# Performance work log

Hardware: AMD Instinct MI355X
Metric: run time of the kernel (lower is better)

Reference implementation:

```python
import jax, jax.numpy as jnp
import numpy as np

EPS_ROT = 1e-6
EPS_FRAME = 1e-8


def make_rotX(angs):
    # angs: [..., 2] (cos-like, sin-like); returns [..., 4, 4]
    n = jnp.sqrt(jnp.sum(angs * angs, axis=-1)) + EPS_ROT
    c = angs[..., 0] / n
    s = angs[..., 1] / n
    z = jnp.zeros_like(c)
    o = jnp.ones_like(c)
    rows = jnp.stack([o, z, z, z,
                      z, c, -s, z,
                      z, s, c, z,
                      z, z, z, o], axis=-1)
    return rows.reshape(c.shape + (4, 4))


def make_rotZ(angs):
    n = jnp.sqrt(jnp.sum(angs * angs, axis=-1)) + EPS_ROT
    c = angs[..., 0] / n
    s = angs[..., 1] / n
    z = jnp.zeros_like(c)
    o = jnp.ones_like(c)
    rows = jnp.stack([c, -s, z, z,
                      s, c, z, z,
                      z, z, o, z,
                      z, z, z, o], axis=-1)
    return rows.reshape(c.shape + (4, 4))


def make_rot_axis(angs, u):
    # Rodrigues rotation about unit axis u, as homogeneous 4x4
    n = jnp.sqrt(jnp.sum(angs * angs, axis=-1)) + EPS_ROT
    ct = angs[..., 0] / n
    st = angs[..., 1] / n
    u0, u1, u2 = u[..., 0], u[..., 1], u[..., 2]
    omc = 1.0 - ct
    z = jnp.zeros_like(ct)
    o = jnp.ones_like(ct)
    rows = jnp.stack([
        ct + u0 * u0 * omc, u0 * u1 * omc - u2 * st, u0 * u2 * omc + u1 * st, z,
        u0 * u1 * omc + u2 * st, ct + u1 * u1 * omc, u1 * u2 * omc - u0 * st, z,
        u0 * u2 * omc - u1 * st, u1 * u2 * omc + u0 * st, ct + u2 * u2 * omc, z,
        z, z, z, o], axis=-1)
    return rows.reshape(ct.shape + (4, 4))


def rigid_from_3_points(N, Ca, C):
    # Gram-Schmidt backbone frame (ideal geometry branch)
    v1 = C - Ca
    v2 = N - Ca
    e1 = v1 / (jnp.linalg.norm(v1, axis=-1, keepdims=True) + EPS_FRAME)
    u2 = v2 - e1 * jnp.sum(e1 * v2, axis=-1, keepdims=True)
    e2 = u2 / (jnp.linalg.norm(u2, axis=-1, keepdims=True) + EPS_FRAME)
    e3 = jnp.cross(e1, e2)
    R = jnp.stack([e1, e2, e3], axis=-1)  # columns -> [B,L,3,3]
    return R, Ca


def _compute(seq, xyz, alphas, base_indices, RTs_in_base_frame, xyzs_in_base_frame):
    B, L = xyz.shape[:2]
    Rs, Ts = rigid_from_3_points(xyz[..., 0, :], xyz[..., 1, :], xyz[..., 2, :])
    top = jnp.concatenate([Rs, Ts[..., None]], axis=-1)  # [B,L,3,4]
    bot = jnp.broadcast_to(jnp.array([0.0, 0.0, 0.0, 1.0], dtype=xyz.dtype), (B, L, 1, 4))
    RTF0 = jnp.concatenate([top, bot], axis=-2)  # [B,L,4,4]

    RT_base = RTs_in_base_frame[seq]  # [B,L,7,4,4]

    RTF1 = RTF0 @ RT_base[:, :, 0] @ make_rotX(alphas[:, :, 0, :])
    RTF2 = RTF0 @ RT_base[:, :, 1] @ make_rotX(alphas[:, :, 1, :])
    RTF3 = RTF0 @ RT_base[:, :, 2] @ make_rotX(alphas[:, :, 2, :])

    basexyzs = xyzs_in_base_frame[seq]  # [B,L,36,4]
    NCr = 0.5 * (basexyzs[:, :, 2, :3] + basexyzs[:, :, 0, :3])
    CAr = basexyzs[:, :, 1, :3]
    CBr = basexyzs[:, :, 4, :3]
    ax1 = jnp.cross(CBr - CAr, NCr - CAr)
    ax1 = ax1 / (jnp.linalg.norm(ax1, axis=-1, keepdims=True) + 1e-8)
    NCp = basexyzs[:, :, 2, :3] - basexyzs[:, :, 0, :3]
    NCpp = NCp - jnp.sum(NCp * NCr, axis=-1, keepdims=True) / jnp.sum(NCr * NCr, axis=-1, keepdims=True) * NCr
    ax2 = jnp.cross(CBr - CAr, NCpp)
    ax2 = ax2 / (jnp.linalg.norm(ax2, axis=-1, keepdims=True) + 1e-8)

    CBrot1 = make_rot_axis(alphas[:, :, 7, :], ax1)
    CBrot2 = make_rot_axis(alphas[:, :, 8, :], ax2)
    RTF8 = RTF0 @ CBrot1 @ CBrot2

    RTF4 = RTF8 @ RT_base[:, :, 3] @ make_rotX(alphas[:, :, 3, :]) @ make_rotZ(alphas[:, :, 9, :])
    RTF5 = RTF4 @ RT_base[:, :, 4] @ make_rotX(alphas[:, :, 4, :])
    RTF6 = RTF5 @ RT_base[:, :, 5] @ make_rotX(alphas[:, :, 5, :])
    RTF7 = RTF6 @ RT_base[:, :, 6] @ make_rotX(alphas[:, :, 6, :])

    RTframes = jnp.stack([RTF0, RTF1, RTF2, RTF3, RTF4, RTF5, RTF6, RTF7, RTF8], axis=2)  # [B,L,9,4,4]

    idx = base_indices[seq]  # [B,L,36], values in [0,9)
    frames = jnp.take_along_axis(RTframes, idx[..., None, None], axis=2)  # [B,L,36,4,4]
    xyzs = jnp.einsum('blaij,blaj->blai', frames, basexyzs)
    return RTframes, xyzs[..., :3]


def setup_inputs() -> dict:
    key = jax.random.key(0)
    ks = jax.random.split(key, 6)
    B, L, NAA, NATOMS = 4, 8192, 80, 36
    seq = jax.random.randint(ks[0], (B, L), 0, NAA)
    xyz = jax.random.normal(ks[1], (B, L, 3, 3), jnp.float32)
    alphas = jax.random.normal(ks[2], (B, L, 10, 2), jnp.float32)
    base_indices = jax.random.randint(ks[3], (NAA, NATOMS), 0, 9)
    xibf = jax.random.normal(ks[4], (NAA, NATOMS, 4), jnp.float32)
    xibf = xibf.at[..., 3].set(1.0)  # homogeneous coords
    RTs = jax.random.normal(ks[5], (NAA, 7, 4, 4), jnp.float32)
    return {"seq": seq, "xyz": xyz, "alphas": alphas, "base_indices": base_indices,
            "RTs_in_base_frame": RTs, "xyzs_in_base_frame": xibf}


def reference(seq, xyz, alphas, base_indices, RTs_in_base_frame, xyzs_in_base_frame):
    return _compute(seq, xyz, alphas, base_indices, RTs_in_base_frame, xyzs_in_base_frame)
```

## Files before the change

kernel.cpp:

```cpp
#include <hip/hip_runtime.h>

#define RPB 64
#define FRS 20
#define RSS (9*FRS)


__device__ __forceinline__ float rsqz(float d) { return rsqrtf(fmaxf(d, 1e-24f)); }

__device__ __forceinline__ void angNorm(float x, float y, float& c, float& s) {
    float inv = rsqz(x*x + y*y);
    c = x * inv; s = y * inv;
}

__device__ __forceinline__ float4 rowMat(const float4 f, const float* __restrict__ B) {
    const float4* q = reinterpret_cast<const float4*>(B);
    float4 b0 = q[0], b1 = q[1], b2 = q[2], b3 = q[3];
    float4 o;
    o.x = f.x*b0.x + f.y*b1.x + f.z*b2.x + f.w*b3.x;
    o.y = f.x*b0.y + f.y*b1.y + f.z*b2.y + f.w*b3.y;
    o.z = f.x*b0.z + f.y*b1.z + f.z*b2.z + f.w*b3.z;
    o.w = f.x*b0.w + f.y*b1.w + f.z*b2.w + f.w*b3.w;
    return o;
}

__device__ __forceinline__ void rotXrow(float4& v, float c, float s) {
    float v1 = v.y, v2 = v.z;
    v.y = c*v1 + s*v2;
    v.z = c*v2 - s*v1;
}

__device__ __forceinline__ void rotZrow(float4& v, float c, float s) {
    float v0 = v.x, v1 = v.y;
    v.x = c*v0 + s*v1;
    v.y = c*v1 - s*v0;
}

__device__ __forceinline__ float4 applyG(const float4 f, const float G[3][3]) {
    float4 o;
    o.x = f.x*G[0][0] + f.y*G[1][0] + f.z*G[2][0];
    o.y = f.x*G[0][1] + f.y*G[1][1] + f.z*G[2][1];
    o.z = f.x*G[0][2] + f.y*G[1][2] + f.z*G[2][2];
    o.w = f.w;
    return o;
}

__device__ __forceinline__ void rotAxis3(float G[3][3], float c, float s,
                                         float u0, float u1, float u2) {
    float omc = 1.0f - c;
    G[0][0] = c + u0*u0*omc;    G[0][1] = u0*u1*omc - u2*s; G[0][2] = u0*u2*omc + u1*s;
    G[1][0] = u0*u1*omc + u2*s; G[1][1] = c + u1*u1*omc;    G[1][2] = u1*u2*omc - u0*s;
    G[2][0] = u0*u2*omc - u1*s; G[2][1] = u1*u2*omc + u0*s; G[2][2] = c + u2*u2*omc;
}


__global__ __launch_bounds__(256, 2) void fused_kernel(
    const int*   __restrict__ seq,
    const float* __restrict__ xyz,
    const float* __restrict__ alphas,
    const int*   __restrict__ bidx,
    const float* __restrict__ RTs,
    const float* __restrict__ xibf,
    float*       __restrict__ out_fr,
    float*       __restrict__ out_xyz,
    int BL)
{
    __shared__ __align__(16) float lds_fr[RPB * RSS];
    __shared__ int lds_seq[RPB];

    const int tid   = threadIdx.x;
    const int lane  = tid & 63;
    const int wv    = tid >> 6;
    const int i     = lane & 3;
    const int res   = wv*16 + (lane >> 2);
    const int base  = blockIdx.x * RPB;
    const int t     = base + res;
    const bool valid = (t < BL);

    float* fl = lds_fr + res * RSS;
    float* fg = out_fr + (size_t)t * 144;

    if (valid) {
        int s = seq[t];
        if (i == 0) lds_seq[res] = s;
        const float* rb = RTs + (size_t)s * 112;
        const float* al = alphas + (size_t)t * 20;

        const float* p = xyz + (size_t)t * 9;
        float N0=p[0], N1=p[1], N2=p[2];
        float A0=p[3], A1=p[4], A2=p[5];
        float C0=p[6], C1=p[7], C2=p[8];
        float v10=C0-A0, v11=C1-A1, v12=C2-A2;
        float v20=N0-A0, v21=N1-A1, v22=N2-A2;
        float i1 = rsqz(v10*v10 + v11*v11 + v12*v12);
        float e10=v10*i1, e11=v11*i1, e12=v12*i1;
        float d  = e10*v20 + e11*v21 + e12*v22;
        float u20=v20-e10*d, u21=v21-e11*d, u22=v22-e12*d;
        float i2 = rsqz(u20*u20 + u21*u21 + u22*u22);
        float e20=u20*i2, e21=u21*i2, e22=u22*i2;
        float e30=e11*e22 - e12*e21;
        float e31=e12*e20 - e10*e22;
        float e32=e10*e21 - e11*e20;

        bool s0 = (i==0), s1 = (i==1), s2 = (i==2);
        float4 f0r;
        f0r.x = s0?e10 : s1?e11 : s2?e12 : 0.f;
        f0r.y = s0?e20 : s1?e21 : s2?e22 : 0.f;
        f0r.z = s0?e30 : s1?e31 : s2?e32 : 0.f;
        f0r.w = s0?A0  : s1?A1  : s2?A2  : 1.f;

        *reinterpret_cast<float4*>(fl + i*4) = f0r;
        *reinterpret_cast<float4*>(fg + i*4) = f0r;

        const float4* a4p = reinterpret_cast<const float4*>(al);
        float4 q0 = a4p[0], q1 = a4p[1], q2 = a4p[2], q3 = a4p[3], q4 = a4p[4];
        float ca0,sa0, ca1,sa1, ca2,sa2, ca3,sa3, ca4,sa4;
        float ca5,sa5, ca6,sa6, ca7,sa7, ca8,sa8, ca9,sa9;
        angNorm(q0.x,q0.y, ca0,sa0);  angNorm(q0.z,q0.w, ca1,sa1);
        angNorm(q1.x,q1.y, ca2,sa2);  angNorm(q1.z,q1.w, ca3,sa3);
        angNorm(q2.x,q2.y, ca4,sa4);  angNorm(q2.z,q2.w, ca5,sa5);
        angNorm(q3.x,q3.y, ca6,sa6);  angNorm(q3.z,q3.w, ca7,sa7);
        angNorm(q4.x,q4.y, ca8,sa8);  angNorm(q4.z,q4.w, ca9,sa9);

        float4 rw;
        rw = rowMat(f0r, rb +  0); rotXrow(rw, ca0, sa0);
        *reinterpret_cast<float4*>(fl + 1*FRS + i*4) = rw;
        *reinterpret_cast<float4*>(fg + 16 + i*4) = rw;
        rw = rowMat(f0r, rb + 16); rotXrow(rw, ca1, sa1);
        *reinterpret_cast<float4*>(fl + 2*FRS + i*4) = rw;
        *reinterpret_cast<float4*>(fg + 32 + i*4) = rw;
        rw = rowMat(f0r, rb + 32); rotXrow(rw, ca2, sa2);
        *reinterpret_cast<float4*>(fl + 3*FRS + i*4) = rw;
        *reinterpret_cast<float4*>(fg + 48 + i*4) = rw;

        const float* bxp = xibf + (size_t)s * 144;
        float4 b0 = reinterpret_cast<const float4*>(bxp)[0];
        float4 b1 = reinterpret_cast<const float4*>(bxp)[1];
        float4 b2 = reinterpret_cast<const float4*>(bxp)[2];
        float4 b4 = reinterpret_cast<const float4*>(bxp)[4];

        float NCr0 = 0.5f*(b2.x + b0.x), NCr1 = 0.5f*(b2.y + b0.y), NCr2 = 0.5f*(b2.z + b0.z);
        float ba0 = b4.x - b1.x, ba1 = b4.y - b1.y, ba2 = b4.z - b1.z;
        float w0 = NCr0 - b1.x, w1 = NCr1 - b1.y, w2 = NCr2 - b1.z;
        float x10 = ba1*w2 - ba2*w1, x11 = ba2*w0 - ba0*w2, x12 = ba0*w1 - ba1*w0;
        float in1 = rsqz(x10*x10 + x11*x11 + x12*x12);
        x10 *= in1; x11 *= in1; x12 *= in1;
        float NCp0 = b2.x - b0.x, NCp1 = b2.y - b0.y, NCp2 = b2.z - b0.z;
        float dp = NCp0*NCr0 + NCp1*NCr1 + NCp2*NCr2;
        float dr = NCr0*NCr0 + NCr1*NCr1 + NCr2*NCr2;
        float sf = dp / dr;
        float g0 = NCp0 - sf*NCr0, g1 = NCp1 - sf*NCr1, g2 = NCp2 - sf*NCr2;
        float x20 = ba1*g2 - ba2*g1, x21 = ba2*g0 - ba0*g2, x22 = ba0*g1 - ba1*g0;
        float in2 = rsqz(x20*x20 + x21*x21 + x22*x22);
        x20 *= in2; x21 *= in2; x22 *= in2;

        float G1[3][3], G2[3][3];
        rotAxis3(G1, ca7, sa7, x10, x11, x12);
        rotAxis3(G2, ca8, sa8, x20, x21, x22);

        float4 f8r = applyG(applyG(f0r, G1), G2);
        *reinterpret_cast<float4*>(fl + 8*FRS + i*4) = f8r;
        *reinterpret_cast<float4*>(fg + 128 + i*4) = f8r;

        rw = rowMat(f8r, rb + 48); rotXrow(rw, ca3, sa3); rotZrow(rw, ca9, sa9);
        *reinterpret_cast<float4*>(fl + 4*FRS + i*4) = rw;
        *reinterpret_cast<float4*>(fg + 64 + i*4) = rw;
        rw = rowMat(rw, rb + 64); rotXrow(rw, ca4, sa4);
        *reinterpret_cast<float4*>(fl + 5*FRS + i*4) = rw;
        *reinterpret_cast<float4*>(fg + 80 + i*4) = rw;
        rw = rowMat(rw, rb + 80); rotXrow(rw, ca5, sa5);
        *reinterpret_cast<float4*>(fl + 6*FRS + i*4) = rw;
        *reinterpret_cast<float4*>(fg + 96 + i*4) = rw;
        rw = rowMat(rw, rb + 96); rotXrow(rw, ca6, sa6);
        *reinterpret_cast<float4*>(fl + 7*FRS + i*4) = rw;
        *reinterpret_cast<float4*>(fg + 112 + i*4) = rw;
    }

    const int wbase = wv * 16;
#pragma unroll
    for (int k = 0; k < 9; ++k) {
        int c = k*64 + lane;
        int lres = c / 36;
        int a = c - lres*36;
        int res2 = wbase + lres;
        int tt = base + res2;
        if (tt < BL) {
            int ss  = lds_seq[res2];
            int idx = bidx[ss*36 + a];
            float4 v = *reinterpret_cast<const float4*>(xibf + ((size_t)ss*36 + a)*4);
            const float* fp = lds_fr + res2*RSS + idx*FRS;
            float4 r0 = *reinterpret_cast<const float4*>(fp);
            float4 r1 = *reinterpret_cast<const float4*>(fp + 4);
            float4 r2 = *reinterpret_cast<const float4*>(fp + 8);
            size_t o = ((size_t)(base + wbase)*36 + c)*3;
            out_xyz[o+0] = r0.x*v.x + r0.y*v.y + r0.z*v.z + r0.w*v.w;
            out_xyz[o+1] = r1.x*v.x + r1.y*v.y + r1.z*v.z + r1.w*v.w;
            out_xyz[o+2] = r2.x*v.x + r2.y*v.y + r2.z*v.z + r2.w*v.w;
        }
    }
}


extern "C" void kernel_launch(void* const* d_in, const int* in_sizes, int n_in,
                              void* d_out, int out_size, void* d_ws, size_t ws_size,
                              hipStream_t stream) {
    const int*   seq    = (const int*)  d_in[0];
    const float* xyz    = (const float*)d_in[1];
    const float* alphas = (const float*)d_in[2];
    const int*   bidx   = (const int*)  d_in[3];
    const float* RTs    = (const float*)d_in[4];
    const float* xibf   = (const float*)d_in[5];
    float*       out    = (float*)d_out;

    int BL = in_sizes[0];
    float* out_xyz = out + (size_t)BL * 144;

    int blocks = (BL + RPB - 1) / RPB;
    fused_kernel<<<blocks, 256, 0, stream>>>(seq, xyz, alphas, bidx, RTs, xibf,
                                             out, out_xyz, BL);
}
```

Measured before the change: 14.53 us.

## Split fused kernel into separate frames and atoms kernels

Breaks the single fused kernel into two launches. The first computes the nine frames per residue and writes them to global memory. The second reads those frames back from global memory (mostly L2) to transform the 36 atoms, one thread per atom. This drops the large LDS staging buffer that limited occupancy and the uneven atom loop, at the cost of an extra launch and a round-trip of the frame data through memory.

```diff
diff --git a/kernel.cpp b/kernel.cpp
--- a/kernel.cpp
+++ b/kernel.cpp
@@ -1,8 +1,4 @@
 #include <hip/hip_runtime.h>
-
-#define RPB 64
-#define FRS 20
-#define RSS (9*FRS)
 
 
 __device__ __forceinline__ float rsqz(float d) { return rsqrtf(fmaxf(d, 1e-24f)); }
@@ -53,150 +49,133 @@
 }
 
 
-__global__ __launch_bounds__(256, 2) void fused_kernel(
+__global__ __launch_bounds__(256, 2) void frames_kernel(
     const int*   __restrict__ seq,
     const float* __restrict__ xyz,
     const float* __restrict__ alphas,
-    const int*   __restrict__ bidx,
     const float* __restrict__ RTs,
     const float* __restrict__ xibf,
     float*       __restrict__ out_fr,
+    int BL)
+{
+    const int tid  = blockIdx.x * 256 + threadIdx.x;
+    const int i    = tid & 3;
+    const int t    = tid >> 2;
+    if (t >= BL) return;
+
+    int s = seq[t];
+    const float* rb = RTs + (size_t)s * 112;
+    const float* al = alphas + (size_t)t * 20;
+    float* fg = out_fr + (size_t)t * 144;
+
+    const float* p = xyz + (size_t)t * 9;
+    float N0=p[0], N1=p[1], N2=p[2];
+    float A0=p[3], A1=p[4], A2=p[5];
+    float C0=p[6], C1=p[7], C2=p[8];
+    float v10=C0-A0, v11=C1-A1, v12=C2-A2;
+    float v20=N0-A0, v21=N1-A1, v22=N2-A2;
+    float i1 = rsqz(v10*v10 + v11*v11 + v12*v12);
+    float e10=v10*i1, e11=v11*i1, e12=v12*i1;
+    float d  = e10*v20 + e11*v21 + e12*v22;
+    float u20=v20-e10*d, u21=v21-e11*d, u22=v22-e12*d;
+    float i2 = rsqz(u20*u20 + u21*u21 + u22*u22);
+    float e20=u20*i2, e21=u21*i2, e22=u22*i2;
+    float e30=e11*e22 - e12*e21;
+    float e31=e12*e20 - e10*e22;
+    float e32=e10*e21 - e11*e20;
+
+    bool s0 = (i==0), s1 = (i==1), s2 = (i==2);
+    float4 f0r;
+    f0r.x = s0?e10 : s1?e11 : s2?e12 : 0.f;
+    f0r.y = s0?e20 : s1?e21 : s2?e22 : 0.f;
+    f0r.z = s0?e30 : s1?e31 : s2?e32 : 0.f;
+    f0r.w = s0?A0  : s1?A1  : s2?A2  : 1.f;
+    *reinterpret_cast<float4*>(fg + i*4) = f0r;
+
+    const float4* a4p = reinterpret_cast<const float4*>(al);
+    float4 q0 = a4p[0], q1 = a4p[1], q2 = a4p[2], q3 = a4p[3], q4 = a4p[4];
+    float ca0,sa0, ca1,sa1, ca2,sa2, ca3,sa3, ca4,sa4;
+    float ca5,sa5, ca6,sa6, ca7,sa7, ca8,sa8, ca9,sa9;
+    angNorm(q0.x,q0.y, ca0,sa0);  angNorm(q0.z,q0.w, ca1,sa1);
+    angNorm(q1.x,q1.y, ca2,sa2);  angNorm(q1.z,q1.w, ca3,sa3);
+    angNorm(q2.x,q2.y, ca4,sa4);  angNorm(q2.z,q2.w, ca5,sa5);
+    angNorm(q3.x,q3.y, ca6,sa6);  angNorm(q3.z,q3.w, ca7,sa7);
+    angNorm(q4.x,q4.y, ca8,sa8);  angNorm(q4.z,q4.w, ca9,sa9);
+
+    float4 rw;
+    rw = rowMat(f0r, rb +  0); rotXrow(rw, ca0, sa0);
+    *reinterpret_cast<float4*>(fg + 16 + i*4) = rw;
+    rw = rowMat(f0r, rb + 16); rotXrow(rw, ca1, sa1);
+    *reinterpret_cast<float4*>(fg + 32 + i*4) = rw;
+    rw = rowMat(f0r, rb + 32); rotXrow(rw, ca2, sa2);
+    *reinterpret_cast<float4*>(fg + 48 + i*4) = rw;
+
+    const float* bxp = xibf + (size_t)s * 144;
+    float4 b0 = reinterpret_cast<const float4*>(bxp)[0];
+    float4 b1 = reinterpret_cast<const float4*>(bxp)[1];
+    float4 b2 = reinterpret_cast<const float4*>(bxp)[2];
+    float4 b4 = reinterpret_cast<const float4*>(bxp)[4];
+
+    float NCr0 = 0.5f*(b2.x + b0.x), NCr1 = 0.5f*(b2.y + b0.y), NCr2 = 0.5f*(b2.z + b0.z);
+    float ba0 = b4.x - b1.x, ba1 = b4.y - b1.y, ba2 = b4.z - b1.z;
+    float w0 = NCr0 - b1.x, w1 = NCr1 - b1.y, w2 = NCr2 - b1.z;
+    float x10 = ba1*w2 - ba2*w1, x11 = ba2*w0 - ba0*w2, x12 = ba0*w1 - ba1*w0;
+    float in1 = rsqz(x10*x10 + x11*x11 + x12*x12);
+    x10 *= in1; x11 *= in1; x12 *= in1;
+    float NCp0 = b2.x - b0.x, NCp1 = b2.y - b0.y, NCp2 = b2.z - b0.z;
+    float dp = NCp0*NCr0 + NCp1*NCr1 + NCp2*NCr2;
+    float dr = NCr0*NCr0 + NCr1*NCr1 + NCr2*NCr2;
+    float sf = dp / dr;
+    float g0 = NCp0 - sf*NCr0, g1 = NCp1 - sf*NCr1, g2 = NCp2 - sf*NCr2;
+    float x20 = ba1*g2 - ba2*g1, x21 = ba2*g0 - ba0*g2, x22 = ba0*g1 - ba1*g0;
+    float in2 = rsqz(x20*x20 + x21*x21 + x22*x22);
+    x20 *= in2; x21 *= in2; x22 *= in2;
+
+    float G1[3][3], G2[3][3];
+    rotAxis3(G1, ca7, sa7, x10, x11, x12);
+    rotAxis3(G2, ca8, sa8, x20, x21, x22);
+
+    float4 f8r = applyG(applyG(f0r, G1), G2);
+    *reinterpret_cast<float4*>(fg + 128 + i*4) = f8r;
+
+    rw = rowMat(f8r, rb + 48); rotXrow(rw, ca3, sa3); rotZrow(rw, ca9, sa9);
+    *reinterpret_cast<float4*>(fg + 64 + i*4) = rw;
+    rw = rowMat(rw, rb + 64); rotXrow(rw, ca4, sa4);
+    *reinterpret_cast<float4*>(fg + 80 + i*4) = rw;
+    rw = rowMat(rw, rb + 80); rotXrow(rw, ca5, sa5);
+    *reinterpret_cast<float4*>(fg + 96 + i*4) = rw;
+    rw = rowMat(rw, rb + 96); rotXrow(rw, ca6, sa6);
+    *reinterpret_cast<float4*>(fg + 112 + i*4) = rw;
+}
+
+
+__global__ __launch_bounds__(256) void atoms_kernel(
+    const int*   __restrict__ seq,
+    const int*   __restrict__ bidx,
+    const float* __restrict__ xibf,
+    const float* __restrict__ frames,
     float*       __restrict__ out_xyz,
     int BL)
 {
-    __shared__ __align__(16) float lds_fr[RPB * RSS];
-    __shared__ int lds_seq[RPB];
-
-    const int tid   = threadIdx.x;
-    const int lane  = tid & 63;
-    const int wv    = tid >> 6;
-    const int i     = lane & 3;
-    const int res   = wv*16 + (lane >> 2);
-    const int base  = blockIdx.x * RPB;
-    const int t     = base + res;
-    const bool valid = (t < BL);
-
-    float* fl = lds_fr + res * RSS;
-    float* fg = out_fr + (size_t)t * 144;
-
-    if (valid) {
-        int s = seq[t];
-        if (i == 0) lds_seq[res] = s;
-        const float* rb = RTs + (size_t)s * 112;
-        const float* al = alphas + (size_t)t * 20;
-
-        const float* p = xyz + (size_t)t * 9;
-        float N0=p[0], N1=p[1], N2=p[2];
-        float A0=p[3], A1=p[4], A2=p[5];
-        float C0=p[6], C1=p[7], C2=p[8];
-        float v10=C0-A0, v11=C1-A1, v12=C2-A2;
-        float v20=N0-A0, v21=N1-A1, v22=N2-A2;
-        float i1 = rsqz(v10*v10 + v11*v11 + v12*v12);
-        float e10=v10*i1, e11=v11*i1, e12=v12*i1;
-        float d  = e10*v20 + e11*v21 + e12*v22;
-        float u20=v20-e10*d, u21=v21-e11*d, u22=v22-e12*d;
-        float i2 = rsqz(u20*u20 + u21*u21 + u22*u22);
-        float e20=u20*i2, e21=u21*i2, e22=u22*i2;
-        float e30=e11*e22 - e12*e21;
-        float e31=e12*e20 - e10*e22;
-        float e32=e10*e21 - e11*e20;
-
-        bool s0 = (i==0), s1 = (i==1), s2 = (i==2);
-        float4 f0r;
-        f0r.x = s0?e10 : s1?e11 : s2?e12 : 0.f;
-        f0r.y = s0?e20 : s1?e21 : s2?e22 : 0.f;
-        f0r.z = s0?e30 : s1?e31 : s2?e32 : 0.f;
-        f0r.w = s0?A0  : s1?A1  : s2?A2  : 1.f;
-
-        *reinterpret_cast<float4*>(fl + i*4) = f0r;
-        *reinterpret_cast<float4*>(fg + i*4) = f0r;
-
-        const float4* a4p = reinterpret_cast<const float4*>(al);
-        float4 q0 = a4p[0], q1 = a4p[1], q2 = a4p[2], q3 = a4p[3], q4 = a4p[4];
-        float ca0,sa0, ca1,sa1, ca2,sa2, ca3,sa3, ca4,sa4;
-        float ca5,sa5, ca6,sa6, ca7,sa7, ca8,sa8, ca9,sa9;
-        angNorm(q0.x,q0.y, ca0,sa0);  angNorm(q0.z,q0.w, ca1,sa1);
-        angNorm(q1.x,q1.y, ca2,sa2);  angNorm(q1.z,q1.w, ca3,sa3);
-        angNorm(q2.x,q2.y, ca4,sa4);  angNorm(q2.z,q2.w, ca5,sa5);
-        angNorm(q3.x,q3.y, ca6,sa6);  angNorm(q3.z,q3.w, ca7,sa7);
-        angNorm(q4.x,q4.y, ca8,sa8);  angNorm(q4.z,q4.w, ca9,sa9);
-
-        float4 rw;
-        rw = rowMat(f0r, rb +  0); rotXrow(rw, ca0, sa0);
-        *reinterpret_cast<float4*>(fl + 1*FRS + i*4) = rw;
-        *reinterpret_cast<float4*>(fg + 16 + i*4) = rw;
-        rw = rowMat(f0r, rb + 16); rotXrow(rw, ca1, sa1);
-        *reinterpret_cast<float4*>(fl + 2*FRS + i*4) = rw;
-        *reinterpret_cast<float4*>(fg + 32 + i*4) = rw;
-        rw = rowMat(f0r, rb + 32); rotXrow(rw, ca2, sa2);
-        *reinterpret_cast<float4*>(fl + 3*FRS + i*4) = rw;
-        *reinterpret_cast<float4*>(fg + 48 + i*4) = rw;
-
-        const float* bxp = xibf + (size_t)s * 144;
-        float4 b0 = reinterpret_cast<const float4*>(bxp)[0];
-        float4 b1 = reinterpret_cast<const float4*>(bxp)[1];
-        float4 b2 = reinterpret_cast<const float4*>(bxp)[2];
-        float4 b4 = reinterpret_cast<const float4*>(bxp)[4];
-
-        float NCr0 = 0.5f*(b2.x + b0.x), NCr1 = 0.5f*(b2.y + b0.y), NCr2 = 0.5f*(b2.z + b0.z);
-        float ba0 = b4.x - b1.x, ba1 = b4.y - b1.y, ba2 = b4.z - b1.z;
-        float w0 = NCr0 - b1.x, w1 = NCr1 - b1.y, w2 = NCr2 - b1.z;
-        float x10 = ba1*w2 - ba2*w1, x11 = ba2*w0 - ba0*w2, x12 = ba0*w1 - ba1*w0;
-        float in1 = rsqz(x10*x10 + x11*x11 + x12*x12);
-        x10 *= in1; x11 *= in1; x12 *= in1;
-        float NCp0 = b2.x - b0.x, NCp1 = b2.y - b0.y, NCp2 = b2.z - b0.z;
-        float dp = NCp0*NCr0 + NCp1*NCr1 + NCp2*NCr2;
-        float dr = NCr0*NCr0 + NCr1*NCr1 + NCr2*NCr2;
-        float sf = dp / dr;
-        float g0 = NCp0 - sf*NCr0, g1 = NCp1 - sf*NCr1, g2 = NCp2 - sf*NCr2;
-        float x20 = ba1*g2 - ba2*g1, x21 = ba2*g0 - ba0*g2, x22 = ba0*g1 - ba1*g0;
-        float in2 = rsqz(x20*x20 + x21*x21 + x22*x22);
-        x20 *= in2; x21 *= in2; x22 *= in2;
-
-        float G1[3][3], G2[3][3];
-        rotAxis3(G1, ca7, sa7, x10, x11, x12);
-        rotAxis3(G2, ca8, sa8, x20, x21, x22);
-
-        float4 f8r = applyG(applyG(f0r, G1), G2);
-        *reinterpret_cast<float4*>(fl + 8*FRS + i*4) = f8r;
-        *reinterpret_cast<float4*>(fg + 128 + i*4) = f8r;
-
-        rw = rowMat(f8r, rb + 48); rotXrow(rw, ca3, sa3); rotZrow(rw, ca9, sa9);
-        *reinterpret_cast<float4*>(fl + 4*FRS + i*4) = rw;
-        *reinterpret_cast<float4*>(fg + 64 + i*4) = rw;
-        rw = rowMat(rw, rb + 64); rotXrow(rw, ca4, sa4);
-        *reinterpret_cast<float4*>(fl + 5*FRS + i*4) = rw;
-        *reinterpret_cast<float4*>(fg + 80 + i*4) = rw;
-        rw = rowMat(rw, rb + 80); rotXrow(rw, ca5, sa5);
-        *reinterpret_cast<float4*>(fl + 6*FRS + i*4) = rw;
-        *reinterpret_cast<float4*>(fg + 96 + i*4) = rw;
-        rw = rowMat(rw, rb + 96); rotXrow(rw, ca6, sa6);
-        *reinterpret_cast<float4*>(fl + 7*FRS + i*4) = rw;
-        *reinterpret_cast<float4*>(fg + 112 + i*4) = rw;
-    }
-
-    const int wbase = wv * 16;
-#pragma unroll
-    for (int k = 0; k < 9; ++k) {
-        int c = k*64 + lane;
-        int lres = c / 36;
-        int a = c - lres*36;
-        int res2 = wbase + lres;
-        int tt = base + res2;
-        if (tt < BL) {
-            int ss  = lds_seq[res2];
-            int idx = bidx[ss*36 + a];
-            float4 v = *reinterpret_cast<const float4*>(xibf + ((size_t)ss*36 + a)*4);
-            const float* fp = lds_fr + res2*RSS + idx*FRS;
-            float4 r0 = *reinterpret_cast<const float4*>(fp);
-            float4 r1 = *reinterpret_cast<const float4*>(fp + 4);
-            float4 r2 = *reinterpret_cast<const float4*>(fp + 8);
-            size_t o = ((size_t)(base + wbase)*36 + c)*3;
-            out_xyz[o+0] = r0.x*v.x + r0.y*v.y + r0.z*v.z + r0.w*v.w;
-            out_xyz[o+1] = r1.x*v.x + r1.y*v.y + r1.z*v.z + r1.w*v.w;
-            out_xyz[o+2] = r2.x*v.x + r2.y*v.y + r2.z*v.z + r2.w*v.w;
-        }
-    }
+    int g = blockIdx.x * 256 + threadIdx.x;
+    if (g >= BL * 36) return;
+    int t = g / 36;
+    int a = g - t * 36;
+    int s = seq[t];
+    int idx = bidx[s * 36 + a];
+
+    const float4* fr = reinterpret_cast<const float4*>(frames + ((size_t)t * 9 + idx) * 16);
+    float4 r0 = fr[0], r1 = fr[1], r2 = fr[2];
+    float4 v  = *reinterpret_cast<const float4*>(xibf + ((size_t)s * 36 + a) * 4);
+
+    float x = r0.x*v.x + r0.y*v.y + r0.z*v.z + r0.w*v.w;
+    float y = r1.x*v.x + r1.y*v.y + r1.z*v.z + r1.w*v.w;
+    float z = r2.x*v.x + r2.y*v.y + r2.z*v.z + r2.w*v.w;
+
+    size_t o = (size_t)g * 3;
+    out_xyz[o+0] = x;
+    out_xyz[o+1] = y;
+    out_xyz[o+2] = z;
 }
 
 
@@ -214,7 +193,9 @@
     int BL = in_sizes[0];
     float* out_xyz = out + (size_t)BL * 144;
 
-    int blocks = (BL + RPB - 1) / RPB;
-    fused_kernel<<<blocks, 256, 0, stream>>>(seq, xyz, alphas, bidx, RTs, xibf,
-                                             out, out_xyz, BL);
-}
+    int blocksA = (BL * 4 + 255) / 256;
+    frames_kernel<<<blocksA, 256, 0, stream>>>(seq, xyz, alphas, RTs, xibf, out, BL);
+
+    int blocksB = (BL * 36 + 255) / 256;
+    atoms_kernel<<<blocksB, 256, 0, stream>>>(seq, bidx, xibf, out, out_xyz, BL);
+}
```

Result: slower. 23.66 us (+62.8%).

## Split block into frame-compute and gather-prefetch warps with block-wide sync

Applied to the files above, without the earlier changes.

Doubles the block to 512 threads. The first four waves compute residue frames into LDS and global memory, while the extra four waves prefetch base indices and base-frame coordinates for the atom stage. After a block-wide barrier, all 512 threads share the per-atom transform, so the index and coordinate loads can overlap the frame math. The cost is a __syncthreads that replaces the old per-wave independence, plus extra registers held by the prefetch waves.

```diff
diff --git a/kernel.cpp b/kernel.cpp
--- a/kernel.cpp
+++ b/kernel.cpp
@@ -53,7 +53,7 @@
 }
 
 
-__global__ __launch_bounds__(256, 2) void fused_kernel(
+__global__ __launch_bounds__(512, 4) void fused_kernel(
     const int*   __restrict__ seq,
     const float* __restrict__ xyz,
     const float* __restrict__ alphas,
@@ -67,134 +67,160 @@
     __shared__ __align__(16) float lds_fr[RPB * RSS];
     __shared__ int lds_seq[RPB];
 
-    const int tid   = threadIdx.x;
-    const int lane  = tid & 63;
-    const int wv    = tid >> 6;
-    const int i     = lane & 3;
-    const int res   = wv*16 + (lane >> 2);
-    const int base  = blockIdx.x * RPB;
-    const int t     = base + res;
-    const bool valid = (t < BL);
-
-    float* fl = lds_fr + res * RSS;
-    float* fg = out_fr + (size_t)t * 144;
-
-    if (valid) {
-        int s = seq[t];
-        if (i == 0) lds_seq[res] = s;
-        const float* rb = RTs + (size_t)s * 112;
-        const float* al = alphas + (size_t)t * 20;
-
-        const float* p = xyz + (size_t)t * 9;
-        float N0=p[0], N1=p[1], N2=p[2];
-        float A0=p[3], A1=p[4], A2=p[5];
-        float C0=p[6], C1=p[7], C2=p[8];
-        float v10=C0-A0, v11=C1-A1, v12=C2-A2;
-        float v20=N0-A0, v21=N1-A1, v22=N2-A2;
-        float i1 = rsqz(v10*v10 + v11*v11 + v12*v12);
-        float e10=v10*i1, e11=v11*i1, e12=v12*i1;
-        float d  = e10*v20 + e11*v21 + e12*v22;
-        float u20=v20-e10*d, u21=v21-e11*d, u22=v22-e12*d;
-        float i2 = rsqz(u20*u20 + u21*u21 + u22*u22);
-        float e20=u20*i2, e21=u21*i2, e22=u22*i2;
-        float e30=e11*e22 - e12*e21;
-        float e31=e12*e20 - e10*e22;
-        float e32=e10*e21 - e11*e20;
-
-        bool s0 = (i==0), s1 = (i==1), s2 = (i==2);
-        float4 f0r;
-        f0r.x = s0?e10 : s1?e11 : s2?e12 : 0.f;
-        f0r.y = s0?e20 : s1?e21 : s2?e22 : 0.f;
-        f0r.z = s0?e30 : s1?e31 : s2?e32 : 0.f;
-        f0r.w = s0?A0  : s1?A1  : s2?A2  : 1.f;
-
-        *reinterpret_cast<float4*>(fl + i*4) = f0r;
-        *reinterpret_cast<float4*>(fg + i*4) = f0r;
-
-        const float4* a4p = reinterpret_cast<const float4*>(al);
-        float4 q0 = a4p[0], q1 = a4p[1], q2 = a4p[2], q3 = a4p[3], q4 = a4p[4];
-        float ca0,sa0, ca1,sa1, ca2,sa2, ca3,sa3, ca4,sa4;
-        float ca5,sa5, ca6,sa6, ca7,sa7, ca8,sa8, ca9,sa9;
-        angNorm(q0.x,q0.y, ca0,sa0);  angNorm(q0.z,q0.w, ca1,sa1);
-        angNorm(q1.x,q1.y, ca2,sa2);  angNorm(q1.z,q1.w, ca3,sa3);
-        angNorm(q2.x,q2.y, ca4,sa4);  angNorm(q2.z,q2.w, ca5,sa5);
-        angNorm(q3.x,q3.y, ca6,sa6);  angNorm(q3.z,q3.w, ca7,sa7);
-        angNorm(q4.x,q4.y, ca8,sa8);  angNorm(q4.z,q4.w, ca9,sa9);
-
-        float4 rw;
-        rw = rowMat(f0r, rb +  0); rotXrow(rw, ca0, sa0);
-        *reinterpret_cast<float4*>(fl + 1*FRS + i*4) = rw;
-        *reinterpret_cast<float4*>(fg + 16 + i*4) = rw;
-        rw = rowMat(f0r, rb + 16); rotXrow(rw, ca1, sa1);
-        *reinterpret_cast<float4*>(fl + 2*FRS + i*4) = rw;
-        *reinterpret_cast<float4*>(fg + 32 + i*4) = rw;
-        rw = rowMat(f0r, rb + 32); rotXrow(rw, ca2, sa2);
-        *reinterpret_cast<float4*>(fl + 3*FRS + i*4) = rw;
-        *reinterpret_cast<float4*>(fg + 48 + i*4) = rw;
-
-        const float* bxp = xibf + (size_t)s * 144;
-        float4 b0 = reinterpret_cast<const float4*>(bxp)[0];
-        float4 b1 = reinterpret_cast<const float4*>(bxp)[1];
-        float4 b2 = reinterpret_cast<const float4*>(bxp)[2];
-        float4 b4 = reinterpret_cast<const float4*>(bxp)[4];
-
-        float NCr0 = 0.5f*(b2.x + b0.x), NCr1 = 0.5f*(b2.y + b0.y), NCr2 = 0.5f*(b2.z + b0.z);
-        float ba0 = b4.x - b1.x, ba1 = b4.y - b1.y, ba2 = b4.z - b1.z;
-        float w0 = NCr0 - b1.x, w1 = NCr1 - b1.y, w2 = NCr2 - b1.z;
-        float x10 = ba1*w2 - ba2*w1, x11 = ba2*w0 - ba0*w2, x12 = ba0*w1 - ba1*w0;
-        float in1 = rsqz(x10*x10 + x11*x11 + x12*x12);
-        x10 *= in1; x11 *= in1; x12 *= in1;
-        float NCp0 = b2.x - b0.x, NCp1 = b2.y - b0.y, NCp2 = b2.z - b0.z;
-        float dp = NCp0*NCr0 + NCp1*NCr1 + NCp2*NCr2;
-        float dr = NCr0*NCr0 + NCr1*NCr1 + NCr2*NCr2;
-        float sf = dp / dr;
-        float g0 = NCp0 - sf*NCr0, g1 = NCp1 - sf*NCr1, g2 = NCp2 - sf*NCr2;
-        float x20 = ba1*g2 - ba2*g1, x21 = ba2*g0 - ba0*g2, x22 = ba0*g1 - ba1*g0;
-        float in2 = rsqz(x20*x20 + x21*x21 + x22*x22);
-        x20 *= in2; x21 *= in2; x22 *= in2;
-
-        float G1[3][3], G2[3][3];
-        rotAxis3(G1, ca7, sa7, x10, x11, x12);
-        rotAxis3(G2, ca8, sa8, x20, x21, x22);
-
-        float4 f8r = applyG(applyG(f0r, G1), G2);
-        *reinterpret_cast<float4*>(fl + 8*FRS + i*4) = f8r;
-        *reinterpret_cast<float4*>(fg + 128 + i*4) = f8r;
-
-        rw = rowMat(f8r, rb + 48); rotXrow(rw, ca3, sa3); rotZrow(rw, ca9, sa9);
-        *reinterpret_cast<float4*>(fl + 4*FRS + i*4) = rw;
-        *reinterpret_cast<float4*>(fg + 64 + i*4) = rw;
-        rw = rowMat(rw, rb + 64); rotXrow(rw, ca4, sa4);
-        *reinterpret_cast<float4*>(fl + 5*FRS + i*4) = rw;
-        *reinterpret_cast<float4*>(fg + 80 + i*4) = rw;
-        rw = rowMat(rw, rb + 80); rotXrow(rw, ca5, sa5);
-        *reinterpret_cast<float4*>(fl + 6*FRS + i*4) = rw;
-        *reinterpret_cast<float4*>(fg + 96 + i*4) = rw;
-        rw = rowMat(rw, rb + 96); rotXrow(rw, ca6, sa6);
-        *reinterpret_cast<float4*>(fl + 7*FRS + i*4) = rw;
-        *reinterpret_cast<float4*>(fg + 112 + i*4) = rw;
+    const int tid  = threadIdx.x;
+    const int lane = tid & 63;
+    const int wv   = tid >> 6;
+    const int base = blockIdx.x * RPB;
+
+    int    pf_idx[5];
+    float4 pf_v[5];
+
+    if (wv < 4) {
+        const int i   = lane & 3;
+        const int res = wv*16 + (lane >> 2);
+        const int t   = base + res;
+        if (t < BL) {
+            int s = seq[t];
+            if (i == 0) lds_seq[res] = s;
+            const float* rb = RTs + (size_t)s * 112;
+            const float* al = alphas + (size_t)t * 20;
+            float* fl = lds_fr + res * RSS;
+            float* fg = out_fr + (size_t)t * 144;
+
+            const float* p = xyz + (size_t)t * 9;
+            float N0=p[0], N1=p[1], N2=p[2];
+            float A0=p[3], A1=p[4], A2=p[5];
+            float C0=p[6], C1=p[7], C2=p[8];
+            float v10=C0-A0, v11=C1-A1, v12=C2-A2;
+            float v20=N0-A0, v21=N1-A1, v22=N2-A2;
+            float i1 = rsqz(v10*v10 + v11*v11 + v12*v12);
+            float e10=v10*i1, e11=v11*i1, e12=v12*i1;
+            float d  = e10*v20 + e11*v21 + e12*v22;
+            float u20=v20-e10*d, u21=v21-e11*d, u22=v22-e12*d;
+            float i2 = rsqz(u20*u20 + u21*u21 + u22*u22);
+            float e20=u20*i2, e21=u21*i2, e22=u22*i2;
+            float e30=e11*e22 - e12*e21;
+            float e31=e12*e20 - e10*e22;
+            float e32=e10*e21 - e11*e20;
+
+            bool c0 = (i==0), c1 = (i==1), c2 = (i==2);
+            float4 f0r;
+            f0r.x = c0?e10 : c1?e11 : c2?e12 : 0.f;
+            f0r.y = c0?e20 : c1?e21 : c2?e22 : 0.f;
+            f0r.z = c0?e30 : c1?e31 : c2?e32 : 0.f;
+            f0r.w = c0?A0  : c1?A1  : c2?A2  : 1.f;
+            *reinterpret_cast<float4*>(fl + i*4) = f0r;
+            *reinterpret_cast<float4*>(fg + i*4) = f0r;
+
+            const float4* a4p = reinterpret_cast<const float4*>(al);
+            float4 q0 = a4p[0], q1 = a4p[1], q2 = a4p[2], q3 = a4p[3], q4 = a4p[4];
+            float ca0,sa0, ca1,sa1, ca2,sa2, ca3,sa3, ca4,sa4;
+            float ca5,sa5, ca6,sa6, ca7,sa7, ca8,sa8, ca9,sa9;
+            angNorm(q0.x,q0.y, ca0,sa0);  angNorm(q0.z,q0.w, ca1,sa1);
+            angNorm(q1.x,q1.y, ca2,sa2);  angNorm(q1.z,q1.w, ca3,sa3);
+            angNorm(q2.x,q2.y, ca4,sa4);  angNorm(q2.z,q2.w, ca5,sa5);
+            angNorm(q3.x,q3.y, ca6,sa6);  angNorm(q3.z,q3.w, ca7,sa7);
+            angNorm(q4.x,q4.y, ca8,sa8);  angNorm(q4.z,q4.w, ca9,sa9);
+
+            float4 rw;
+            rw = rowMat(f0r, rb +  0); rotXrow(rw, ca0, sa0);
+            *reinterpret_cast<float4*>(fl + 1*FRS + i*4) = rw;
+            *reinterpret_cast<float4*>(fg + 16 + i*4) = rw;
+            rw = rowMat(f0r, rb + 16); rotXrow(rw, ca1, sa1);
+            *reinterpret_cast<float4*>(fl + 2*FRS + i*4) = rw;
+            *reinterpret_cast<float4*>(fg + 32 + i*4) = rw;
+            rw = rowMat(f0r, rb + 32); rotXrow(rw, ca2, sa2);
+            *reinterpret_cast<float4*>(fl + 3*FRS + i*4) = rw;
+            *reinterpret_cast<float4*>(fg + 48 + i*4) = rw;
+
+            const float* bxp = xibf + (size_t)s * 144;
+            float4 b0 = reinterpret_cast<const float4*>(bxp)[0];
+            float4 b1 = reinterpret_cast<const float4*>(bxp)[1];
+            float4 b2 = reinterpret_cast<const float4*>(bxp)[2];
+            float4 b4 = reinterpret_cast<const float4*>(bxp)[4];
+
+            float NCr0 = 0.5f*(b2.x + b0.x), NCr1 = 0.5f*(b2.y + b0.y), NCr2 = 0.5f*(b2.z + b0.z);
+            float ba0 = b4.x - b1.x, ba1 = b4.y - b1.y, ba2 = b4.z - b1.z;
+            float w0 = NCr0 - b1.x, w1 = NCr1 - b1.y, w2 = NCr2 - b1.z;
+            float x10 = ba1*w2 - ba2*w1, x11 = ba2*w0 - ba0*w2, x12 = ba0*w1 - ba1*w0;
+            float in1 = rsqz(x10*x10 + x11*x11 + x12*x12);
+            x10 *= in1; x11 *= in1; x12 *= in1;
+            float NCp0 = b2.x - b0.x, NCp1 = b2.y - b0.y, NCp2 = b2.z - b0.z;
+            float dp = NCp0*NCr0 + NCp1*NCr1 + NCp2*NCr2;
+            float dr = NCr0*NCr0 + NCr1*NCr1 + NCr2*NCr2;
+            float sf = dp / dr;
+            float g0 = NCp0 - sf*NCr0, g1 = NCp1 - sf*NCr1, g2 = NCp2 - sf*NCr2;
+            float x20 = ba1*g2 - ba2*g1, x21 = ba2*g0 - ba0*g2, x22 = ba0*g1 - ba1*g0;
+            float in2 = rsqz(x20*x20 + x21*x21 + x22*x22);
+            x20 *= in2; x21 *= in2; x22 *= in2;
+
+            float G1[3][3], G2[3][3];
+            rotAxis3(G1, ca7, sa7, x10, x11, x12);
+            rotAxis3(G2, ca8, sa8, x20, x21, x22);
+
+            float4 f8r = applyG(applyG(f0r, G1), G2);
+            *reinterpret_cast<float4*>(fl + 8*FRS + i*4) = f8r;
+            *reinterpret_cast<float4*>(fg + 128 + i*4) = f8r;
+
+            rw = rowMat(f8r, rb + 48); rotXrow(rw, ca3, sa3); rotZrow(rw, ca9, sa9);
+            *reinterpret_cast<float4*>(fl + 4*FRS + i*4) = rw;
+            *reinterpret_cast<float4*>(fg + 64 + i*4) = rw;
+            rw = rowMat(rw, rb + 64); rotXrow(rw, ca4, sa4);
+            *reinterpret_cast<float4*>(fl + 5*FRS + i*4) = rw;
+            *reinterpret_cast<float4*>(fg + 80 + i*4) = rw;
+            rw = rowMat(rw, rb + 80); rotXrow(rw, ca5, sa5);
+            *reinterpret_cast<float4*>(fl + 6*FRS + i*4) = rw;
+            *reinterpret_cast<float4*>(fg + 96 + i*4) = rw;
+            rw = rowMat(rw, rb + 96); rotXrow(rw, ca6, sa6);
+            *reinterpret_cast<float4*>(fl + 7*FRS + i*4) = rw;
+            *reinterpret_cast<float4*>(fg + 112 + i*4) = rw;
+        }
+    } else {
+#pragma unroll
+        for (int k = 0; k < 5; ++k) {
+            int c = tid + k*512;
+            pf_idx[k] = 0;
+            pf_v[k] = make_float4(0.f, 0.f, 0.f, 0.f);
+            if (c < RPB*36) {
+                int res = c / 36;
+                int a = c - res*36;
+                int tt = base + res;
+                if (tt < BL) {
+                    int ss = seq[tt];
+                    pf_idx[k] = bidx[ss*36 + a];
+                    pf_v[k]   = *reinterpret_cast<const float4*>(xibf + ((size_t)ss*36 + a)*4);
+                }
+            }
+        }
     }
-
-    const int wbase = wv * 16;
+    __syncthreads();
+
 #pragma unroll
-    for (int k = 0; k < 9; ++k) {
-        int c = k*64 + lane;
-        int lres = c / 36;
-        int a = c - lres*36;
-        int res2 = wbase + lres;
-        int tt = base + res2;
-        if (tt < BL) {
-            int ss  = lds_seq[res2];
-            int idx = bidx[ss*36 + a];
-            float4 v = *reinterpret_cast<const float4*>(xibf + ((size_t)ss*36 + a)*4);
-            const float* fp = lds_fr + res2*RSS + idx*FRS;
-            float4 r0 = *reinterpret_cast<const float4*>(fp);
-            float4 r1 = *reinterpret_cast<const float4*>(fp + 4);
-            float4 r2 = *reinterpret_cast<const float4*>(fp + 8);
-            size_t o = ((size_t)(base + wbase)*36 + c)*3;
-            out_xyz[o+0] = r0.x*v.x + r0.y*v.y + r0.z*v.z + r0.w*v.w;
-            out_xyz[o+1] = r1.x*v.x + r1.y*v.y + r1.z*v.z + r1.w*v.w;
-            out_xyz[o+2] = r2.x*v.x + r2.y*v.y + r2.z*v.z + r2.w*v.w;
+    for (int k = 0; k < 5; ++k) {
+        int c = tid + k*512;
+        if (c < RPB*36) {
+            int res = c / 36;
+            int a = c - res*36;
+            int tt = base + res;
+            if (tt < BL) {
+                int idx; float4 v;
+                if (wv >= 4) {
+                    idx = pf_idx[k];
+                    v   = pf_v[k];
+                } else {
+                    int ss = lds_seq[res];
+                    idx = bidx[ss*36 + a];
+                    v   = *reinterpret_cast<const float4*>(xibf + ((size_t)ss*36 + a)*4);
+                }
+                const float* fp = lds_fr + res*RSS + idx*FRS;
+                float4 r0 = *reinterpret_cast<const float4*>(fp);
+                float4 r1 = *reinterpret_cast<const float4*>(fp + 4);
+                float4 r2 = *reinterpret_cast<const float4*>(fp + 8);
+                size_t o = ((size_t)base*36 + c)*3;
+                out_xyz[o+0] = r0.x*v.x + r0.y*v.y + r0.z*v.z + r0.w*v.w;
+                out_xyz[o+1] = r1.x*v.x + r1.y*v.y + r1.z*v.z + r1.w*v.w;
+                out_xyz[o+2] = r2.x*v.x + r2.y*v.y + r2.z*v.z + r2.w*v.w;
+            }
         }
     }
 }
@@ -215,6 +241,6 @@
     float* out_xyz = out + (size_t)BL * 144;
 
     int blocks = (BL + RPB - 1) / RPB;
-    fused_kernel<<<blocks, 256, 0, stream>>>(seq, xyz, alphas, bidx, RTs, xibf,
+    fused_kernel<<<blocks, 512, 0, stream>>>(seq, xyz, alphas, bidx, RTs, xibf,
                                              out, out_xyz, BL);
 }
```

After: 17.45 us. 1.2x slower.
